# Performance work log

Hardware: AMD Instinct MI355X
Metric: run time of the kernel (lower is better)

## Reference

```python
import jax, jax.numpy as jnp
import numpy as np

# dims: b=2, n=1024 windows, seq_ref=1, seq_in=16, nh_in=4 (seq_in*nh_in=64),
# nv=4 variables, nc=32 channels, n_lon=n_lat=4 Gaussian basis offsets
B, N, SR, SI, NH, NV, NC, NLON, NLAT = 2, 1024, 1, 16, 4, 4, 32, 4, 4
MIN_SIGMA = 1e-10


def setup_inputs() -> dict:
    key = jax.random.key(0)
    k1, k2, k3 = jax.random.split(key, 3)
    x = jax.random.normal(k1, (B, N, SR, SI * NH, NV, NC), dtype=jnp.float32)
    coords_lon = jax.random.normal(k2, (B, N, SR, SI, NH), dtype=jnp.float32)
    coords_lat = jax.random.normal(k3, (B, N, SR, SI, NH), dtype=jnp.float32)
    # mus are linspace(-grid_dist_out, grid_dist_out, n) in the torch module
    mus_lon = jnp.linspace(-1.0, 1.0, NLON).astype(jnp.float32)
    mus_lat = jnp.linspace(-1.0, 1.0, NLAT).astype(jnp.float32)
    sigma = jnp.full((1,), 0.5, dtype=jnp.float32)  # grid min_dist, learnable scalar
    return dict(x=x, coords_lon=coords_lon, coords_lat=coords_lat,
                mus_lon=mus_lon, mus_lat=mus_lat, sigma=sigma)


def reference(x, coords_lon, coords_lat, mus_lon, mus_lat, sigma):
    # x: (b,n,seq_ref,seq_in*nh_in,nv,nc); coords_*: (b,n,seq_ref,seq_in,nh_in)
    b, n, sr, si, nh = coords_lon.shape
    nv, nc = x.shape[-2:]
    nlon, nlat = mus_lon.shape[0], mus_lat.shape[0]
    sig = jnp.maximum(sigma, MIN_SIGMA)  # clamp(min=min_sigma)
    # Gaussian kernels over relative lon/lat distances
    wlon = jnp.exp(-0.5 * ((coords_lon[..., None] - mus_lon) / sig) ** 2)  # (b,n,sr,si,nh,Lo)
    wlat = jnp.exp(-0.5 * ((coords_lat[..., None] - mus_lat) / sig) ** 2)  # (b,n,sr,si,nh,La)
    # outer product over (Lo, La); flatten (seq_in, nh_in) -> s
    w = (wlon[..., :, None] * wlat[..., None, :]).reshape(b, n, sr, si * nh, nlon, nlat)
    # normalize over the neighbor axis (dim=3). weights are nv-independent
    # (torch repeat_interleaves over nv; broadcasting is equivalent)
    w = w / jnp.sum(w, axis=3, keepdims=True)
    # weighted neighbor aggregation: sum over s
    out = jnp.einsum('bnrsvc,bnrsxy->bnrvxyc', x, w)  # (b,n,sr,nv,Lo,La,nc)
    return out.reshape(b, n * sr, nv, nlon, nlat, nc)
```

## Files before the change

### kernel.cpp

```cpp
#include <hip/hip_runtime.h>
#include <hip/hip_bf16.h>

#define NWIN 2048
#define SDIM 64
#define NJ 16

__device__ __forceinline__ float bf2f(unsigned int u16) {
    union { unsigned int i; float f; } v;
    v.i = u16 << 16;
    return v.f;
}

__global__ __launch_bounds__(256, 4) void gauss_agg_kernel(
    const void* __restrict__ x,
    const void* __restrict__ clon,
    const void* __restrict__ clat,
    const void* __restrict__ mlon,
    const void* __restrict__ mlat,
    const void* __restrict__ sigma,
    float* __restrict__ out)
{
    __shared__ alignas(16) float s_wlon[SDIM][4];
    __shared__ alignas(16) float s_wlat[SDIM][4];
    __shared__ float s_sinv[NJ];
    __shared__ int s_flags;

    const int tid = threadIdx.x;
    const int win = blockIdx.x;

    if (tid == 0) {
        const unsigned short* px = (const unsigned short*)x;
        const unsigned short* pc = (const unsigned short*)clon;
        int vx = 0, vc = 0;
#pragma unroll
        for (int i = 0; i < 16; ++i) {
            const int ex = (px[2 * i] >> 7) & 0xFF;
            vx += (ex >= 102 && ex <= 134);
            const int ec = (pc[2 * i] >> 7) & 0xFF;
            vc += (ec >= 102 && ec <= 134);
        }
        int f = 0;
        if (vx >= 12) f |= 1;
        if (vc >= 12) f |= 2;
        if (((const unsigned short*)mlon)[0] != 0) f |= 4;
        if (((const unsigned short*)sigma)[0] != 0) f |= 8;
        s_flags = f;
    }
    __syncthreads();
    const int flags = s_flags;
    const bool xb = flags & 1, cb = flags & 2, mb = flags & 4, sb = flags & 8;

    if (tid < 64) {
        const int lane = tid;
        const float sigraw = sb ? bf2f(((const unsigned short*)sigma)[0])
                                : ((const float*)sigma)[0];
        const float inv = 1.0f / fmaxf(sigraw, 1e-10f);

        float mlo[4], mla[4];
#pragma unroll
        for (int l = 0; l < 4; ++l) {
            mlo[l] = mb ? bf2f(((const unsigned short*)mlon)[l])
                        : ((const float*)mlon)[l];
            mla[l] = mb ? bf2f(((const unsigned short*)mlat)[l])
                        : ((const float*)mlat)[l];
        }

        float lon, lat;
        if (cb) {
            lon = bf2f(((const unsigned short*)clon)[win * SDIM + lane]);
            lat = bf2f(((const unsigned short*)clat)[win * SDIM + lane]);
        } else {
            lon = ((const float*)clon)[win * SDIM + lane];
            lat = ((const float*)clat)[win * SDIM + lane];
        }

        float wlon[4], wlat[4];
#pragma unroll
        for (int l = 0; l < 4; ++l) {
            const float dlo = (lon - mlo[l]) * inv;
            wlon[l] = __expf(-0.5f * dlo * dlo);
            const float dla = (lat - mla[l]) * inv;
            wlat[l] = __expf(-0.5f * dla * dla);
        }
        *reinterpret_cast<float4*>(&s_wlon[lane][0]) =
            make_float4(wlon[0], wlon[1], wlon[2], wlon[3]);
        *reinterpret_cast<float4*>(&s_wlat[lane][0]) =
            make_float4(wlat[0], wlat[1], wlat[2], wlat[3]);

        float p[NJ];
#pragma unroll
        for (int lo = 0; lo < 4; ++lo)
#pragma unroll
            for (int la = 0; la < 4; ++la)
                p[lo * 4 + la] = wlon[lo] * wlat[la];
#pragma unroll
        for (int j = 0; j < NJ; ++j) {
            float v = p[j];
#pragma unroll
            for (int off = 1; off < 64; off <<= 1)
                v += __shfl_xor(v, off, 64);
            p[j] = v;
        }
        if (lane == 0) {
#pragma unroll
            for (int j = 0; j < NJ; ++j)
                s_sinv[j] = 1.0f / p[j];
        }
    }
    __syncthreads();

    const int v    = tid >> 6;
    const int lane = tid & 63;
    const int sh   = lane >> 4;
    const int c2   = lane & 15;

    const float4* wl4 = reinterpret_cast<const float4*>(&s_wlon[0][0]);
    const float4* wt4 = reinterpret_cast<const float4*>(&s_wlat[0][0]);

    float acc0[NJ], acc1[NJ];
#pragma unroll
    for (int j = 0; j < NJ; ++j) { acc0[j] = 0.0f; acc1[j] = 0.0f; }

    const size_t base = (size_t)win * 4096 + v * 16 + c2;

    if (xb) {
        const unsigned int* xp = (const unsigned int*)x + base;
#pragma unroll 4
        for (int it = 0; it < 16; ++it) {
            const int s = 4 * it + sh;
            const unsigned int u = xp[(size_t)s * 64];
            union { unsigned int i; float fl; } u0, u1;
            u0.i = u << 16;
            u1.i = u & 0xffff0000u;
            const float f0 = u0.fl, f1 = u1.fl;
            const float4 wl = wl4[s];
            const float4 wt = wt4[s];
            const float wlv[4] = { wl.x, wl.y, wl.z, wl.w };
            const float wtv[4] = { wt.x, wt.y, wt.z, wt.w };
            float t0[4], t1[4];
#pragma unroll
            for (int la = 0; la < 4; ++la) { t0[la] = f0 * wtv[la]; t1[la] = f1 * wtv[la]; }
#pragma unroll
            for (int lo = 0; lo < 4; ++lo)
#pragma unroll
                for (int la = 0; la < 4; ++la) {
                    acc0[lo * 4 + la] += wlv[lo] * t0[la];
                    acc1[lo * 4 + la] += wlv[lo] * t1[la];
                }
        }
    } else {
        const float2* xp = (const float2*)x + base;
#pragma unroll 4
        for (int it = 0; it < 16; ++it) {
            const int s = 4 * it + sh;
            const float2 xv = xp[(size_t)s * 64];
            const float f0 = xv.x, f1 = xv.y;
            const float4 wl = wl4[s];
            const float4 wt = wt4[s];
            const float wlv[4] = { wl.x, wl.y, wl.z, wl.w };
            const float wtv[4] = { wt.x, wt.y, wt.z, wt.w };
            float t0[4], t1[4];
#pragma unroll
            for (int la = 0; la < 4; ++la) { t0[la] = f0 * wtv[la]; t1[la] = f1 * wtv[la]; }
#pragma unroll
            for (int lo = 0; lo < 4; ++lo)
#pragma unroll
                for (int la = 0; la < 4; ++la) {
                    acc0[lo * 4 + la] += wlv[lo] * t0[la];
                    acc1[lo * 4 + la] += wlv[lo] * t1[la];
                }
        }
    }

#pragma unroll
    for (int j = 0; j < NJ; ++j) {
        float a = acc0[j], b = acc1[j];
        a += __shfl_xor(a, 16, 64);
        a += __shfl_xor(a, 32, 64);
        b += __shfl_xor(b, 16, 64);
        b += __shfl_xor(b, 32, 64);
        acc0[j] = a; acc1[j] = b;
    }

    if (sh == 0) {
        float2* op = reinterpret_cast<float2*>(out);
#pragma unroll
        for (int j = 0; j < NJ; ++j) {
            const float si = s_sinv[j];
            op[((size_t)(win * 4 + v) * NJ + j) * 16 + c2] =
                make_float2(acc0[j] * si, acc1[j] * si);
        }
    }
}

extern "C" void kernel_launch(void* const* d_in, const int* in_sizes, int n_in,
                              void* d_out, int out_size, void* d_ws, size_t ws_size,
                              hipStream_t stream) {
    dim3 grid(NWIN);
    dim3 block(256);
    gauss_agg_kernel<<<grid, block, 0, stream>>>(
        d_in[0], d_in[1], d_in[2], d_in[3], d_in[4], d_in[5],
        (float*)d_out);
}
```

Before: 115.0 us.

## Prefetch x before weight computation and probe dtype per thread

Removes the single-thread dtype-flag setup and its extra barrier: each thread now probes the input dtype itself with vectorized loads. The first half of the x loads for each thread is issued before the Gaussian weight and normalization phase, and the second half right after the barrier, so global memory latency overlaps the weight computation. The main loop is fully unrolled over register-held values. This raises register pressure (16 prefetched values plus 32 accumulators) and makes every thread read the probe bytes redundantly.

```diff
diff --git a/kernel.cpp b/kernel.cpp
--- a/kernel.cpp
+++ b/kernel.cpp
@@ -9,6 +9,23 @@
     union { unsigned int i; float f; } v;
     v.i = u16 << 16;
     return v.f;
+}
+
+__device__ __forceinline__ int bf16ish(unsigned int w) {
+    const int e = (w >> 7) & 0xFF;
+    return (e >= 102 && e <= 134) ? 1 : 0;
+}
+
+__device__ __forceinline__ bool probe_bf16(const void* p) {
+    const uint4* q = (const uint4*)p;
+    int v = 0;
+#pragma unroll
+    for (int i = 0; i < 4; ++i) {
+        const uint4 w = q[i];
+        v += bf16ish(w.x); v += bf16ish(w.y);
+        v += bf16ish(w.z); v += bf16ish(w.w);
+    }
+    return v >= 12;
 }
 
 __global__ __launch_bounds__(256, 4) void gauss_agg_kernel(
@@ -23,35 +40,34 @@
     __shared__ alignas(16) float s_wlon[SDIM][4];
     __shared__ alignas(16) float s_wlat[SDIM][4];
     __shared__ float s_sinv[NJ];
-    __shared__ int s_flags;
-
-    const int tid = threadIdx.x;
-    const int win = blockIdx.x;
-
-    if (tid == 0) {
-        const unsigned short* px = (const unsigned short*)x;
-        const unsigned short* pc = (const unsigned short*)clon;
-        int vx = 0, vc = 0;
-#pragma unroll
-        for (int i = 0; i < 16; ++i) {
-            const int ex = (px[2 * i] >> 7) & 0xFF;
-            vx += (ex >= 102 && ex <= 134);
-            const int ec = (pc[2 * i] >> 7) & 0xFF;
-            vc += (ec >= 102 && ec <= 134);
-        }
-        int f = 0;
-        if (vx >= 12) f |= 1;
-        if (vc >= 12) f |= 2;
-        if (((const unsigned short*)mlon)[0] != 0) f |= 4;
-        if (((const unsigned short*)sigma)[0] != 0) f |= 8;
-        s_flags = f;
-    }
-    __syncthreads();
-    const int flags = s_flags;
-    const bool xb = flags & 1, cb = flags & 2, mb = flags & 4, sb = flags & 8;
+
+    const int tid  = threadIdx.x;
+    const int win  = blockIdx.x;
+    const int v    = tid >> 6;
+    const int lane = tid & 63;
+    const int sh   = lane >> 4;
+    const int c2   = lane & 15;
+
+    const bool xb = probe_bf16(x);
+
+    const size_t base = (size_t)win * 4096 + v * 16 + c2;
+    unsigned int ua[8];
+    float2 fa[8];
+    if (xb) {
+        const unsigned int* xp = (const unsigned int*)x + base;
+#pragma unroll
+        for (int it = 0; it < 8; ++it) ua[it] = xp[(size_t)(4 * it + sh) * 64];
+    } else {
+        const float2* xp = (const float2*)x + base;
+#pragma unroll
+        for (int it = 0; it < 8; ++it) fa[it] = xp[(size_t)(4 * it + sh) * 64];
+    }
 
     if (tid < 64) {
-        const int lane = tid;
+        const bool cb = probe_bf16(clon);
+        const bool mb = ((const unsigned short*)mlon)[0] != 0;
+        const bool sb = ((const unsigned short*)sigma)[0] != 0;
+
         const float sigraw = sb ? bf2f(((const unsigned short*)sigma)[0])
                                 : ((const float*)sigma)[0];
         const float inv = 1.0f / fmaxf(sigraw, 1e-10f);
@@ -67,11 +83,11 @@
 
         float lon, lat;
         if (cb) {
-            lon = bf2f(((const unsigned short*)clon)[win * SDIM + lane]);
-            lat = bf2f(((const unsigned short*)clat)[win * SDIM + lane]);
+            lon = bf2f(((const unsigned short*)clon)[win * SDIM + tid]);
+            lat = bf2f(((const unsigned short*)clat)[win * SDIM + tid]);
         } else {
-            lon = ((const float*)clon)[win * SDIM + lane];
-            lat = ((const float*)clat)[win * SDIM + lane];
+            lon = ((const float*)clon)[win * SDIM + tid];
+            lat = ((const float*)clat)[win * SDIM + tid];
         }
 
         float wlon[4], wlat[4];
@@ -82,9 +98,9 @@
             const float dla = (lat - mla[l]) * inv;
             wlat[l] = __expf(-0.5f * dla * dla);
         }
-        *reinterpret_cast<float4*>(&s_wlon[lane][0]) =
+        *reinterpret_cast<float4*>(&s_wlon[tid][0]) =
             make_float4(wlon[0], wlon[1], wlon[2], wlon[3]);
-        *reinterpret_cast<float4*>(&s_wlat[lane][0]) =
+        *reinterpret_cast<float4*>(&s_wlat[tid][0]) =
             make_float4(wlat[0], wlat[1], wlat[2], wlat[3]);
 
         float p[NJ];
@@ -95,13 +111,13 @@
                 p[lo * 4 + la] = wlon[lo] * wlat[la];
 #pragma unroll
         for (int j = 0; j < NJ; ++j) {
-            float v = p[j];
+            float t = p[j];
 #pragma unroll
             for (int off = 1; off < 64; off <<= 1)
-                v += __shfl_xor(v, off, 64);
-            p[j] = v;
-        }
-        if (lane == 0) {
+                t += __shfl_xor(t, off, 64);
+            p[j] = t;
+        }
+        if (tid == 0) {
 #pragma unroll
             for (int j = 0; j < NJ; ++j)
                 s_sinv[j] = 1.0f / p[j];
@@ -109,11 +125,6 @@
     }
     __syncthreads();
 
-    const int v    = tid >> 6;
-    const int lane = tid & 63;
-    const int sh   = lane >> 4;
-    const int c2   = lane & 15;
-
     const float4* wl4 = reinterpret_cast<const float4*>(&s_wlon[0][0]);
     const float4* wt4 = reinterpret_cast<const float4*>(&s_wlat[0][0]);
 
@@ -121,14 +132,17 @@
 #pragma unroll
     for (int j = 0; j < NJ; ++j) { acc0[j] = 0.0f; acc1[j] = 0.0f; }
 
-    const size_t base = (size_t)win * 4096 + v * 16 + c2;
-
     if (xb) {
         const unsigned int* xp = (const unsigned int*)x + base;
-#pragma unroll 4
+        unsigned int ub[8];
+#pragma unroll
+        for (int it = 0; it < 8; ++it)
+            ub[it] = xp[(size_t)(4 * (it + 8) + sh) * 64];
+
+#pragma unroll
         for (int it = 0; it < 16; ++it) {
+            const unsigned int u = (it < 8) ? ua[it] : ub[it - 8];
             const int s = 4 * it + sh;
-            const unsigned int u = xp[(size_t)s * 64];
             union { unsigned int i; float fl; } u0, u1;
             u0.i = u << 16;
             u1.i = u & 0xffff0000u;
@@ -150,10 +164,15 @@
         }
     } else {
         const float2* xp = (const float2*)x + base;
-#pragma unroll 4
+        float2 fb[8];
+#pragma unroll
+        for (int it = 0; it < 8; ++it)
+            fb[it] = xp[(size_t)(4 * (it + 8) + sh) * 64];
+
+#pragma unroll
         for (int it = 0; it < 16; ++it) {
+            const float2 xv = (it < 8) ? fa[it] : fb[it - 8];
             const int s = 4 * it + sh;
-            const float2 xv = xp[(size_t)s * 64];
             const float f0 = xv.x, f1 = xv.y;
             const float4 wl = wl4[s];
             const float4 wt = wt4[s];
```

After: 151.8 us. +31.9%, slower.
